# Performance work log

Measured on AMD Instinct MI355X. Metric: run time of the kernel, lower is better.

The kernel has to match this reference:

```python
import jax, jax.numpy as jnp
import numpy as np

D = 256; NH = 8; NL = 4; NP = 4; DH = D // NH; FF = 1024; B = 2
SHAPES = np.array([[112, 112], [56, 56], [28, 28], [14, 14]], np.int32)  # (H_l, W_l)
SIZES = (SHAPES[:, 0] * SHAPES[:, 1]).astype(np.int64)
STARTS = np.concatenate([[0], np.cumsum(SIZES)])
S = int(SIZES.sum())


def setup_inputs() -> dict:
    key = jax.random.key(0)
    ks = jax.random.split(key, 10)
    def w(k, shape, s=0.02):
        return (s * jax.random.normal(k, shape)).astype(jnp.float32)
    z = lambda *sh: jnp.zeros(sh, jnp.float32)
    return dict(
        src=w(ks[0], (B, S, D), 1.0),
        pos=w(ks[1], (B, S, D), 1.0),
        reference_points=jax.random.uniform(ks[2], (B, S, NL, 2), jnp.float32),
        spatial_shapes=jnp.asarray(SHAPES),
        level_start_index=jnp.asarray(STARTS[:-1].astype(np.int32)),
        W_off=w(ks[3], (D, NH * NL * NP * 2)), b_off=z(NH * NL * NP * 2),
        W_attn=w(ks[4], (D, NH * NL * NP)), b_attn=z(NH * NL * NP),
        W_val=w(ks[5], (D, D)), b_val=z(D),
        W_out=w(ks[6], (D, D)), b_out=z(D),
        g1=jnp.ones((D,), jnp.float32), be1=z(D),
        g2=jnp.ones((D,), jnp.float32), be2=z(D),
        W1=w(ks[7], (D, FF)), b1=z(FF),
        W2=w(ks[8], (FF, D)), b2=z(D),
    )


def _ln(x, g, b):
    m = x.mean(-1, keepdims=True)
    v = ((x - m) ** 2).mean(-1, keepdims=True)
    return (x - m) * jax.lax.rsqrt(v + 1e-5) * g + b


def _bilinear(value, Hl, Wl, loc):
    # value: [B, NH, Hl*Wl, DH]; loc: [B, S, NH, NP, 2] in [0,1] (x,y)
    # grid_sample semantics: align_corners=False, padding_mode='zeros'
    b, s = loc.shape[0], loc.shape[1]
    x = loc[..., 0] * Wl - 0.5
    y = loc[..., 1] * Hl - 0.5
    x0 = jnp.floor(x); y0 = jnp.floor(y)
    dx = x - x0; dy = y - y0
    out = jnp.zeros((b, s, NH, NP, DH), value.dtype)
    corners = ((x0, y0, (1 - dx) * (1 - dy)), (x0 + 1, y0, dx * (1 - dy)),
               (x0, y0 + 1, (1 - dx) * dy), (x0 + 1, y0 + 1, dx * dy))
    for cx, cy, wgt in corners:
        valid = (cx >= 0) & (cx < Wl) & (cy >= 0) & (cy < Hl)
        idx = (jnp.clip(cy, 0, Hl - 1) * Wl + jnp.clip(cx, 0, Wl - 1)).astype(jnp.int32)
        idx = idx.transpose(0, 2, 1, 3).reshape(b, NH, s * NP)  # [B,NH,S*NP]
        v = jnp.take_along_axis(value, idx[..., None], axis=2)   # [B,NH,S*NP,DH]
        v = v.reshape(b, NH, s, NP, DH).transpose(0, 2, 1, 3, 4)  # [B,S,NH,NP,DH]
        out = out + v * (wgt * valid.astype(value.dtype))[..., None]
    return out


def _msda(query, src, ref, W_off, b_off, W_attn, b_attn, W_val, b_val, W_out, b_out):
    b, s, _ = query.shape
    value = src @ W_val + b_val                                   # [B,S,D]
    off = (query @ W_off + b_off).reshape(b, s, NH, NL, NP, 2)
    aw = jax.nn.softmax((query @ W_attn + b_attn).reshape(b, s, NH, NL * NP), axis=-1)
    aw = aw.reshape(b, s, NH, NL, NP)
    wh = jnp.asarray(SHAPES[:, ::-1].astype(np.float32))          # [L,2] as (W,H)
    loc = ref[:, :, None, :, None, :] + off / wh[None, None, None, :, None, :]
    out = jnp.zeros((b, s, NH, DH), value.dtype)
    for l in range(NL):
        Hl, Wl = int(SHAPES[l, 0]), int(SHAPES[l, 1])
        v_l = value[:, STARTS[l]:STARTS[l + 1]].reshape(b, Hl * Wl, NH, DH)
        v_l = v_l.transpose(0, 2, 1, 3)                           # [B,NH,HW,DH]
        samp = _bilinear(v_l, Hl, Wl, loc[:, :, :, l])            # [B,S,NH,NP,DH]
        out = out + jnp.einsum('bshp,bshpd->bshd', aw[:, :, :, l], samp)
    return out.reshape(b, s, D) @ W_out + b_out


def reference(src, pos, reference_points, spatial_shapes, level_start_index,
              W_off, b_off, W_attn, b_attn, W_val, b_val, W_out, b_out,
              g1, be1, g2, be2, W1, b1, W2, b2):
    q = src + pos
    src2 = _msda(q, src, reference_points, W_off, b_off, W_attn, b_attn,
                 W_val, b_val, W_out, b_out)
    x = _ln(src + src2, g1, be1)
    f = jnp.maximum(x @ W1 + b1, 0.0) @ W2 + b2
    return _ln(x + f, g2, be2)
```

## Files before the change

kernel.cpp:

```cpp
#include <hip/hip_runtime.h>

constexpr int D_   = 256;
constexpr int NH_  = 8;
constexpr int DH_  = 32;
constexpr int NL_  = 4;
constexpr int NP_  = 4;
constexpr int FF_  = 1024;
constexpr int B_   = 2;
constexpr int S_   = 16660;
constexpr int NR_  = B_ * S_;

typedef __attribute__((ext_vector_type(8))) short bf16x8;
typedef __attribute__((ext_vector_type(4))) float f32x4;

__device__ __forceinline__ ushort f2bf(float f) {
  unsigned u = __float_as_uint(f);
  return (ushort)((u + 0x7FFFu + ((u >> 16) & 1u)) >> 16);
}

__global__ __launch_bounds__(256)
void prep_kernel(const float* __restrict__ src, const float* __restrict__ pos,
                 ushort* __restrict__ qb, ushort* __restrict__ srcb, int n4) {
  int i = blockIdx.x * 256 + threadIdx.x;
  if (i >= n4) return;
  float4 s = ((const float4*)src)[i];
  float4 p = ((const float4*)pos)[i];
  ushort4 sb = {f2bf(s.x), f2bf(s.y), f2bf(s.z), f2bf(s.w)};
  ushort4 q  = {f2bf(s.x + p.x), f2bf(s.y + p.y), f2bf(s.z + p.z), f2bf(s.w + p.w)};
  ((ushort4*)srcb)[i] = sb;
  ((ushort4*)qb)[i]   = q;
}

__global__ __launch_bounds__(256)
void cvt_weights(const float* __restrict__ Woff, const float* __restrict__ Wattn,
                 const float* __restrict__ Wval, const float* __restrict__ Wout,
                 const float* __restrict__ W1,  const float* __restrict__ W2,
                 ushort* __restrict__ out) {
  const int wi = blockIdx.y;
  const int i = blockIdx.x * 256 + threadIdx.x;
  const float* src; int K, N; size_t off;
  switch (wi) {
    case 0: src = Woff;  K = 256;  N = 256;  off = 0;      break;
    case 1: src = Wattn; K = 256;  N = 128;  off = 65536;  break;
    case 2: src = Wval;  K = 256;  N = 256;  off = 98304;  break;
    case 3: src = Wout;  K = 256;  N = 256;  off = 163840; break;
    case 4: src = W1;    K = 256;  N = 1024; off = 229376; break;
    default:src = W2;    K = 1024; N = 256;  off = 491520; break;
  }
  if (i >= K * N) return;
  int k = i / N, n = i - k * N;
  out[off + (size_t)n * K + k] = f2bf(src[i]);
}

template<bool RELU, bool OUTBF16>
__global__ __launch_bounds__(256, 2)
void gemm_mfma(const ushort* __restrict__ A, const ushort* __restrict__ Wt,
               const float* __restrict__ bias, void* __restrict__ Cout,
               int M, int N, int K) {
  __shared__ ushort As[128 * 32];
  __shared__ ushort Bs[128 * 32];
  const int tid = threadIdx.x;
  const int l = tid & 63, w = tid >> 6;
  const int brow = blockIdx.x * 128, bcol = blockIdx.y * 128;

  const int rA0 = w * 32 + (l >> 2);
  const int kbl = (l & 3) ^ ((rA0 >> 1) & 3);
  const ushort* agp0 = A  + (size_t)(brow + rA0)      * K + kbl * 8;
  const ushort* agp1 = A  + (size_t)(brow + rA0 + 16) * K + kbl * 8;
  const ushort* bgp0 = Wt + (size_t)(bcol + rA0)      * K + kbl * 8;
  const ushort* bgp1 = Wt + (size_t)(bcol + rA0 + 16) * K + kbl * 8;
  ushort* asl0 = As + w * 1024; ushort* asl1 = asl0 + 512;
  ushort* bsl0 = Bs + w * 1024; ushort* bsl1 = bsl0 + 512;

  const int l15 = l & 15;
  const int kg  = l >> 4;
  const int swz = (l15 >> 1) & 3;
  const int rbase = (w & 1) * 64, cbase = (w >> 1) * 64;
  const int aoff = (rbase + l15) * 32 + ((kg ^ swz) * 8);
  const int boff = (cbase + l15) * 32 + ((kg ^ swz) * 8);

  f32x4 acc[4][4];
#pragma unroll
  for (int i = 0; i < 4; ++i)
#pragma unroll
    for (int j = 0; j < 4; ++j) acc[i][j] = (f32x4){0.f, 0.f, 0.f, 0.f};

  for (int bk = 0; bk < K; bk += 32) {
    __builtin_amdgcn_global_load_lds(
        (const __attribute__((address_space(1))) void*)(agp0 + bk),
        (__attribute__((address_space(3))) void*)asl0, 16, 0, 0);
    __builtin_amdgcn_global_load_lds(
        (const __attribute__((address_space(1))) void*)(agp1 + bk),
        (__attribute__((address_space(3))) void*)asl1, 16, 0, 0);
    __builtin_amdgcn_global_load_lds(
        (const __attribute__((address_space(1))) void*)(bgp0 + bk),
        (__attribute__((address_space(3))) void*)bsl0, 16, 0, 0);
    __builtin_amdgcn_global_load_lds(
        (const __attribute__((address_space(1))) void*)(bgp1 + bk),
        (__attribute__((address_space(3))) void*)bsl1, 16, 0, 0);
    __syncthreads();

    bf16x8 af[4], bfr[4];
#pragma unroll
    for (int i = 0; i < 4; ++i) af[i]  = *(const bf16x8*)(As + aoff + i * 512);
#pragma unroll
    for (int j = 0; j < 4; ++j) bfr[j] = *(const bf16x8*)(Bs + boff + j * 512);
#pragma unroll
    for (int i = 0; i < 4; ++i)
#pragma unroll
      for (int j = 0; j < 4; ++j)
        acc[i][j] = __builtin_amdgcn_mfma_f32_16x16x32_bf16(af[i], bfr[j], acc[i][j], 0, 0, 0);
    __syncthreads();
  }

  const int r0 = kg * 4;
#pragma unroll
  for (int j = 0; j < 4; ++j) {
    const int col = bcol + cbase + j * 16 + l15;
    const float bj = bias[col];
#pragma unroll
    for (int i = 0; i < 4; ++i) {
      const int rowb = brow + rbase + i * 16 + r0;
#pragma unroll
      for (int r = 0; r < 4; ++r) {
        const int row = rowb + r;
        if (row < M) {
          float v = acc[i][j][r] + bj;
          if (RELU) v = fmaxf(v, 0.f);
          if (OUTBF16) ((ushort*)Cout)[(size_t)row * N + col] = f2bf(v);
          else         ((float*)Cout)[(size_t)row * N + col]  = v;
        }
      }
    }
  }
}

__global__ __launch_bounds__(256)
void msda_kernel(const ushort* __restrict__ value, const float* __restrict__ offs,
                 const float* __restrict__ attn, const float* __restrict__ ref,
                 ushort* __restrict__ out) {
  __shared__ int4   descI[4 * 136];
  __shared__ float4 descW[4 * 136];
  const int t = threadIdx.x;
  const int n0 = blockIdx.x * 4;

  const int Hs[4] = {112, 56, 28, 14};
  const int st[4] = {0, 12544, 15680, 16464};

#pragma unroll
  for (int rep = 0; rep < 2; ++rep) {
    const int di = t + rep * 256;
    const int q = di >> 7, h = (di >> 4) & 7, lp = di & 15;
    const int lv = lp >> 2;
    const int n = n0 + q;

    float lg = attn[(size_t)n * 128 + h * 16 + lp];
    float mx = lg;
#pragma unroll
    for (int o = 8; o; o >>= 1) mx = fmaxf(mx, __shfl_xor(mx, o, 64));
    float e = __expf(lg - mx);
    float ssum = e;
#pragma unroll
    for (int o = 8; o; o >>= 1) ssum += __shfl_xor(ssum, o, 64);
    const float aw = e / ssum;

    const int Hl = Hs[lv], Wl = Hs[lv];
    const float fS = (float)Wl;
    const float refx = ref[((size_t)n * 4 + lv) * 2 + 0];
    const float refy = ref[((size_t)n * 4 + lv) * 2 + 1];
    const float ox = offs[(size_t)n * 256 + h * 32 + lp * 2 + 0];
    const float oy = offs[(size_t)n * 256 + h * 32 + lp * 2 + 1];
    float x = fmaf(refx, fS, ox) - 0.5f;
    float y = fmaf(refy, fS, oy) - 0.5f;
    float x0f = floorf(x), y0f = floorf(y);
    float dx = x - x0f, dy = y - y0f;
    int x0 = (int)x0f, y0 = (int)y0f;
    int x0c = min(max(x0, 0), Wl - 1), x1c = min(max(x0 + 1, 0), Wl - 1);
    int y0c = min(max(y0, 0), Hl - 1), y1c = min(max(y0 + 1, 0), Hl - 1);
    bool vx0 = (x0 >= 0) && (x0 < Wl), vx1 = (x0 + 1 >= 0) && (x0 + 1 < Wl);
    bool vy0 = (y0 >= 0) && (y0 < Hl), vy1 = (y0 + 1 >= 0) && (y0 + 1 < Hl);
    int4 I;
    I.x = st[lv] + y0c * Wl + x0c;
    I.y = st[lv] + y0c * Wl + x1c;
    I.z = st[lv] + y1c * Wl + x0c;
    I.w = st[lv] + y1c * Wl + x1c;
    float4 Wv;
    Wv.x = (1.f - dx) * (1.f - dy) * ((vx0 && vy0) ? aw : 0.f);
    Wv.y = dx * (1.f - dy)         * ((vx1 && vy0) ? aw : 0.f);
    Wv.z = (1.f - dx) * dy         * ((vx0 && vy1) ? aw : 0.f);
    Wv.w = dx * dy                 * ((vx1 && vy1) ? aw : 0.f);
    const int slot = q * 136 + h * 17 + lp;
    descI[slot] = I;
    descW[slot] = Wv;
  }
  __syncthreads();

  const int q = t >> 6, lane = t & 63;
  const int h = lane >> 3, c = lane & 7;
  const int n = n0 + q;
  const int b = n / S_;
  const ushort* base = value + (size_t)b * S_ * 256 + h * 32 + c * 4;

  float a0 = 0.f, a1 = 0.f, a2 = 0.f, a3 = 0.f;
#pragma unroll
  for (int pt = 0; pt < 16; ++pt) {
    const int slot = q * 136 + h * 17 + pt;
    int4 I = descI[slot];
    float4 Wv = descW[slot];
    int   Ia[4] = {I.x, I.y, I.z, I.w};
    float Wa[4] = {Wv.x, Wv.y, Wv.z, Wv.w};
#pragma unroll
    for (int cr = 0; cr < 4; ++cr) {
      uint2 u = *(const uint2*)(base + (size_t)Ia[cr] * 256);
      float f0 = __uint_as_float(u.x << 16);
      float f1 = __uint_as_float(u.x & 0xffff0000u);
      float f2 = __uint_as_float(u.y << 16);
      float f3 = __uint_as_float(u.y & 0xffff0000u);
      a0 = fmaf(Wa[cr], f0, a0);
      a1 = fmaf(Wa[cr], f1, a1);
      a2 = fmaf(Wa[cr], f2, a2);
      a3 = fmaf(Wa[cr], f3, a3);
    }
  }
  ushort4 o = {f2bf(a0), f2bf(a1), f2bf(a2), f2bf(a3)};
  *(ushort4*)(out + (size_t)n * 256 + h * 32 + c * 4) = o;
}

template<bool WB>
__global__ __launch_bounds__(256)
void add_ln_kernel(const float* __restrict__ a, const float* __restrict__ r,
                   const float* __restrict__ g, const float* __restrict__ be,
                   float* __restrict__ out, ushort* __restrict__ outb, int M) {
  const int wave = threadIdx.x >> 6;
  const int lane = threadIdx.x & 63;
  const int row = blockIdx.x * 4 + wave;
  if (row >= M) return;
  const float4 av = *(const float4*)(a + (size_t)row * 256 + lane * 4);
  const float4 rv = *(const float4*)(r + (size_t)row * 256 + lane * 4);
  float4 v = {av.x + rv.x, av.y + rv.y, av.z + rv.z, av.w + rv.w};
  float s  = v.x + v.y + v.z + v.w;
  float s2 = v.x * v.x + v.y * v.y + v.z * v.z + v.w * v.w;
#pragma unroll
  for (int o = 32; o > 0; o >>= 1) {
    s  += __shfl_xor(s, o, 64);
    s2 += __shfl_xor(s2, o, 64);
  }
  const float mean = s * (1.f / 256.f);
  const float var  = s2 * (1.f / 256.f) - mean * mean;
  const float rstd = rsqrtf(var + 1e-5f);
  const float4 gv = *(const float4*)(g + lane * 4);
  const float4 bv = *(const float4*)(be + lane * 4);
  float4 o4;
  o4.x = (v.x - mean) * rstd * gv.x + bv.x;
  o4.y = (v.y - mean) * rstd * gv.y + bv.y;
  o4.z = (v.z - mean) * rstd * gv.z + bv.z;
  o4.w = (v.w - mean) * rstd * gv.w + bv.w;
  *(float4*)(out + (size_t)row * 256 + lane * 4) = o4;
  if (WB) {
    ushort4 ob = {f2bf(o4.x), f2bf(o4.y), f2bf(o4.z), f2bf(o4.w)};
    ((ushort4*)(outb + (size_t)row * 256))[lane] = ob;
  }
}

extern "C" void kernel_launch(void* const* d_in, const int* in_sizes, int n_in,
                              void* d_out, int out_size, void* d_ws, size_t ws_size,
                              hipStream_t stream) {
  const float* src    = (const float*)d_in[0];
  const float* pos    = (const float*)d_in[1];
  const float* refpts = (const float*)d_in[2];
  const float* W_off  = (const float*)d_in[5];
  const float* b_off  = (const float*)d_in[6];
  const float* W_attn = (const float*)d_in[7];
  const float* b_attn = (const float*)d_in[8];
  const float* W_val  = (const float*)d_in[9];
  const float* b_val  = (const float*)d_in[10];
  const float* W_out  = (const float*)d_in[11];
  const float* b_out  = (const float*)d_in[12];
  const float* g1     = (const float*)d_in[13];
  const float* be1    = (const float*)d_in[14];
  const float* g2     = (const float*)d_in[15];
  const float* be2    = (const float*)d_in[16];
  const float* W1     = (const float*)d_in[17];
  const float* b1     = (const float*)d_in[18];
  const float* W2     = (const float*)d_in[19];
  const float* b2     = (const float*)d_in[20];
  float* out = (float*)d_out;

  const size_t NF = (size_t)NR_ * 256;
  char* p = (char*)d_ws;
  ushort* qb   = (ushort*)p; p += NF * 2;
  ushort* srcb = (ushort*)p; p += NF * 2;
  ushort* valb = (ushort*)p; p += NF * 2;
  float*  offs = (float*) p; p += NF * 4;
  float*  attn = (float*) p; p += NF * 2;
  float*  tmp  = (float*) p; p += NF * 4;
  float*  x    = (float*) p; p += NF * 4;
  ushort* Wt   = (ushort*)p; p += 753664 * 2;
  ushort* msdab = srcb;
  ushort* xb    = qb;
  ushort* hid   = valb;
  ushort* WtOff  = Wt;
  ushort* WtAttn = Wt + 65536;
  ushort* WtVal  = Wt + 98304;
  ushort* WtOut  = Wt + 163840;
  ushort* Wt1    = Wt + 229376;
  ushort* Wt2    = Wt + 491520;

  dim3 blk(256);
  const int n4 = NR_ * 64;
  const int gr = (NR_ + 127) / 128;

  prep_kernel<<<(n4 + 255) / 256, blk, 0, stream>>>(src, pos, qb, srcb, n4);
  cvt_weights<<<dim3(1024, 6), blk, 0, stream>>>(W_off, W_attn, W_val, W_out, W1, W2, Wt);
  gemm_mfma<false, true ><<<dim3(gr, 2), blk, 0, stream>>>(srcb, WtVal, b_val, valb, NR_, 256, 256);
  gemm_mfma<false, false><<<dim3(gr, 2), blk, 0, stream>>>(qb, WtOff, b_off, offs, NR_, 256, 256);
  gemm_mfma<false, false><<<dim3(gr, 1), blk, 0, stream>>>(qb, WtAttn, b_attn, attn, NR_, 128, 256);
  msda_kernel<<<NR_ / 4, blk, 0, stream>>>(valb, offs, attn, refpts, msdab);
  gemm_mfma<false, false><<<dim3(gr, 2), blk, 0, stream>>>(msdab, WtOut, b_out, tmp, NR_, 256, 256);
  add_ln_kernel<true ><<<(NR_ + 3) / 4, blk, 0, stream>>>(tmp, src, g1, be1, x, xb, NR_);
  gemm_mfma<true,  true ><<<dim3(gr, 8), blk, 0, stream>>>(xb, Wt1, b1, hid, NR_, 1024, 256);
  gemm_mfma<false, false><<<dim3(gr, 2), blk, 0, stream>>>(hid, Wt2, b2, tmp, NR_, 256, 1024);
  add_ln_kernel<false><<<(NR_ + 3) / 4, blk, 0, stream>>>(tmp, x, g2, be2, out, nullptr, NR_);
}
```

Measured before the change: 442.4 us.

## Add K=256 GEMM with full-panel LDS weights, fuse offset/attn GEMMs, remap MSDA blocks

Adds a GEMM kernel for K=256 that keeps each lane's whole A row slice in registers and loads the full 128x256 weight panel into LDS in one go with direct global-to-LDS loads and an XOR swizzle. The inner loop therefore has no k-loop barriers. It is used for the value, output, FFN1 and a fused offset+attention projection; the weight buffer is reordered so Woff and Wattn are contiguous and one 384-column launch fills both outputs. The MSDA kernel also remaps block IDs so each XCD handles a contiguous range of queries, aiming for better L2 locality. The trade-offs are 64 KB of LDS per block and high register use, which may limit occupancy.

```diff
diff --git a/kernel.cpp b/kernel.cpp
--- a/kernel.cpp
+++ b/kernel.cpp
@@ -40,9 +40,9 @@
   const int i = blockIdx.x * 256 + threadIdx.x;
   const float* src; int K, N; size_t off;
   switch (wi) {
-    case 0: src = Woff;  K = 256;  N = 256;  off = 0;      break;
-    case 1: src = Wattn; K = 256;  N = 128;  off = 65536;  break;
-    case 2: src = Wval;  K = 256;  N = 256;  off = 98304;  break;
+    case 0: src = Wval;  K = 256;  N = 256;  off = 0;      break;
+    case 1: src = Woff;  K = 256;  N = 256;  off = 65536;  break;
+    case 2: src = Wattn; K = 256;  N = 128;  off = 131072; break;
     case 3: src = Wout;  K = 256;  N = 256;  off = 163840; break;
     case 4: src = W1;    K = 256;  N = 1024; off = 229376; break;
     default:src = W2;    K = 1024; N = 256;  off = 491520; break;
@@ -50,6 +50,95 @@
   if (i >= K * N) return;
   int k = i / N, n = i - k * N;
   out[off + (size_t)n * K + k] = f2bf(src[i]);
+}
+
+template<int MODE>
+__global__ __launch_bounds__(256, 2)
+void gemm_blds(const ushort* __restrict__ A, const ushort* __restrict__ Wpan,
+               const float* __restrict__ bias, const float* __restrict__ bias2,
+               void* __restrict__ C, void* __restrict__ C2, int M, int Ns) {
+  __shared__ ushort Bs[128 * 256];
+  const int tid = threadIdx.x;
+  const int l = tid & 63, w = tid >> 6;
+  const int l15 = l & 15, kg = l >> 4;
+  const int cxor = l15 & 7;
+  const int bx = blockIdx.x, by = blockIdx.y;
+
+  const int r0 = bx * 128 + w * 16 + l15;
+  const int r1 = r0 + 64;
+  const int r0c = min(r0, M - 1), r1c = min(r1, M - 1);
+  const ushort* a0p = A + (size_t)r0c * 256 + kg * 8;
+  const ushort* a1p = A + (size_t)r1c * 256 + kg * 8;
+  bf16x8 a0[8], a1[8];
+#pragma unroll
+  for (int kk = 0; kk < 8; ++kk) a0[kk] = *(const bf16x8*)(a0p + kk * 32);
+#pragma unroll
+  for (int kk = 0; kk < 8; ++kk) a1[kk] = *(const bf16x8*)(a1p + kk * 32);
+
+  const ushort* wp = Wpan + (size_t)by * 128 * 256;
+#pragma unroll
+  for (int rnd = 0; rnd < 16; ++rnd) {
+    int gi = rnd * 256 + tid;
+    int col = gi >> 5;
+    int gphys = gi & 31;
+    int glog = gphys ^ (col & 7);
+    __builtin_amdgcn_global_load_lds(
+        (const __attribute__((address_space(1))) void*)(wp + (size_t)col * 256 + glog * 8),
+        (__attribute__((address_space(3))) void*)(Bs + (size_t)(rnd * 256 + w * 64) * 8),
+        16, 0, 0);
+  }
+
+  float bj[8];
+#pragma unroll
+  for (int ct = 0; ct < 8; ++ct) {
+    int colg = by * 128 + ct * 16 + l15;
+    if (MODE == 3) bj[ct] = (colg < 256) ? bias[colg] : bias2[colg - 256];
+    else           bj[ct] = bias[colg];
+  }
+
+  __syncthreads();
+
+  f32x4 acc0[8], acc1[8];
+#pragma unroll
+  for (int ct = 0; ct < 8; ++ct) {
+    acc0[ct] = (f32x4){0.f, 0.f, 0.f, 0.f};
+    acc1[ct] = (f32x4){0.f, 0.f, 0.f, 0.f};
+  }
+#pragma unroll
+  for (int ct = 0; ct < 8; ++ct) {
+    const int cb = (ct * 16 + l15) * 256;
+#pragma unroll
+    for (int kk = 0; kk < 8; ++kk) {
+      bf16x8 b = *(const bf16x8*)(Bs + cb + (((kk * 4 + kg) ^ cxor) * 8));
+      acc0[ct] = __builtin_amdgcn_mfma_f32_16x16x32_bf16(a0[kk], b, acc0[ct], 0, 0, 0);
+      acc1[ct] = __builtin_amdgcn_mfma_f32_16x16x32_bf16(a1[kk], b, acc1[ct], 0, 0, 0);
+    }
+  }
+
+  const int orow0 = bx * 128 + w * 16 + kg * 4;
+#pragma unroll
+  for (int sl = 0; sl < 2; ++sl) {
+    const int rowb = orow0 + sl * 64;
+#pragma unroll
+    for (int ct = 0; ct < 8; ++ct) {
+      const int colg = by * 128 + ct * 16 + l15;
+#pragma unroll
+      for (int r = 0; r < 4; ++r) {
+        const int row = rowb + r;
+        if (row >= M) continue;
+        float v = (sl ? acc1[ct][r] : acc0[ct][r]) + bj[ct];
+        if (MODE == 2) v = fmaxf(v, 0.f);
+        if (MODE == 3) {
+          if (colg < 256) ((float*)C )[(size_t)row * 256 + colg]       = v;
+          else            ((float*)C2)[(size_t)row * 128 + (colg-256)] = v;
+        } else if (MODE == 0) {
+          ((float*)C)[(size_t)row * Ns + colg] = v;
+        } else {
+          ((ushort*)C)[(size_t)row * Ns + colg] = f2bf(v);
+        }
+      }
+    }
+  }
 }
 
 template<bool RELU, bool OUTBF16>
@@ -142,7 +231,10 @@
   __shared__ int4   descI[4 * 136];
   __shared__ float4 descW[4 * 136];
   const int t = threadIdx.x;
-  const int n0 = blockIdx.x * 4;
+  const int orig = blockIdx.x;
+  const int xcd = orig & 7, ii = orig >> 3;
+  const int wg = (xcd < 2 ? xcd * 1042 : 2 * 1042 + (xcd - 2) * 1041) + ii;
+  const int n0 = wg * 4;
 
   const int Hs[4] = {112, 56, 28, 14};
   const int st[4] = {0, 12544, 15680, 16464};
@@ -299,12 +391,11 @@
   ushort* msdab = srcb;
   ushort* xb    = qb;
   ushort* hid   = valb;
-  ushort* WtOff  = Wt;
-  ushort* WtAttn = Wt + 65536;
-  ushort* WtVal  = Wt + 98304;
-  ushort* WtOut  = Wt + 163840;
-  ushort* Wt1    = Wt + 229376;
-  ushort* Wt2    = Wt + 491520;
+  ushort* WtVal = Wt;
+  ushort* WtOA  = Wt + 65536;
+  ushort* WtOut = Wt + 163840;
+  ushort* Wt1   = Wt + 229376;
+  ushort* Wt2   = Wt + 491520;
 
   dim3 blk(256);
   const int n4 = NR_ * 64;
@@ -312,13 +403,16 @@
 
   prep_kernel<<<(n4 + 255) / 256, blk, 0, stream>>>(src, pos, qb, srcb, n4);
   cvt_weights<<<dim3(1024, 6), blk, 0, stream>>>(W_off, W_attn, W_val, W_out, W1, W2, Wt);
-  gemm_mfma<false, true ><<<dim3(gr, 2), blk, 0, stream>>>(srcb, WtVal, b_val, valb, NR_, 256, 256);
-  gemm_mfma<false, false><<<dim3(gr, 2), blk, 0, stream>>>(qb, WtOff, b_off, offs, NR_, 256, 256);
-  gemm_mfma<false, false><<<dim3(gr, 1), blk, 0, stream>>>(qb, WtAttn, b_attn, attn, NR_, 128, 256);
+  gemm_blds<1><<<dim3(gr, 2), blk, 0, stream>>>(srcb, WtVal, b_val, nullptr,
+                                                valb, nullptr, NR_, 256);
+  gemm_blds<3><<<dim3(gr, 3), blk, 0, stream>>>(qb, WtOA, b_off, b_attn,
+                                                offs, attn, NR_, 0);
   msda_kernel<<<NR_ / 4, blk, 0, stream>>>(valb, offs, attn, refpts, msdab);
-  gemm_mfma<false, false><<<dim3(gr, 2), blk, 0, stream>>>(msdab, WtOut, b_out, tmp, NR_, 256, 256);
+  gemm_blds<0><<<dim3(gr, 2), blk, 0, stream>>>(msdab, WtOut, b_out, nullptr,
+                                                tmp, nullptr, NR_, 256);
   add_ln_kernel<true ><<<(NR_ + 3) / 4, blk, 0, stream>>>(tmp, src, g1, be1, x, xb, NR_);
-  gemm_mfma<true,  true ><<<dim3(gr, 8), blk, 0, stream>>>(xb, Wt1, b1, hid, NR_, 1024, 256);
+  gemm_blds<2><<<dim3(gr, 8), blk, 0, stream>>>(xb, Wt1, b1, nullptr,
+                                                hid, nullptr, NR_, 1024);
   gemm_mfma<false, false><<<dim3(gr, 2), blk, 0, stream>>>(hid, Wt2, b2, tmp, NR_, 256, 1024);
   add_ln_kernel<false><<<(NR_ + 3) / 4, blk, 0, stream>>>(tmp, x, g2, be2, out, nullptr, NR_);
 }
```

After: 410.6 us. 7.2% less time.
